# Performance work log

Measured on AMD Instinct MI355X. Metric: run time of the kernel, lower is better.

## Reference

```python
import jax, jax.numpy as jnp
import numpy as np

GROUP_SIZE = 128


def _unpack_int4(packed):
    # packed: [..., P] int32, each holding 8 int4 nibbles (LSB-first).
    u = jax.lax.bitcast_convert_type(packed, jnp.uint32)
    shifts = jnp.arange(8, dtype=jnp.uint32) * 4  # nibble bit offsets
    vals = (u[..., None] >> shifts) & jnp.uint32(15)  # [..., P, 8]
    return vals.reshape(*packed.shape[:-1], -1)  # [..., P*8] in [0, 15]


def setup_inputs() -> dict:
    key = jax.random.key(0)
    k1, k2, k3, k4 = jax.random.split(key, 4)
    B, S, K, O = 4, 16, 4096, 11008
    G = K // GROUP_SIZE          # 32 groups
    GP = (G + 7) // 8            # 4 packed-zero columns
    imax = np.iinfo(np.int32).max
    x = jax.random.normal(k1, (B, S, K), dtype=jnp.float16)
    qweight_i32 = jax.random.randint(k2, (O, K // 8), 0, imax, dtype=jnp.int32)
    qzeros_i32 = jax.random.randint(k3, (O, GP), 0, imax, dtype=jnp.int32)
    scales_f16 = jax.random.uniform(k4, (O, G), dtype=jnp.float16,
                                    minval=0.001, maxval=0.02)
    return {"x": x, "qweight_i32": qweight_i32, "qzeros_i32": qzeros_i32,
            "scales_f16": scales_f16}


def reference(x, qweight_i32, qzeros_i32, scales_f16):
    O, G = scales_f16.shape
    K = G * GROUP_SIZE
    # Dequantize: w = (q - z) * s, per-group int4 quantization.
    q = _unpack_int4(qweight_i32)[:, :K].astype(jnp.float16)       # [O, K]
    z = _unpack_int4(qzeros_i32)[:, :G].astype(jnp.float16)        # [O, G]
    z_k = jnp.repeat(z, GROUP_SIZE, axis=1)                        # [O, K]
    s_k = jnp.repeat(scales_f16, GROUP_SIZE, axis=1)               # [O, K]
    w = (q - z_k) * s_k                                            # fp16 [O, K]
    x2d = x.reshape(-1, K).astype(jnp.float16)                     # [m, K]
    out = jnp.matmul(x2d, w.T).astype(jnp.float32)                 # [m, O]
    return out.reshape(*x.shape[:-1], O)
```

## Files before the change

### kernel.cpp

```cpp
#include <hip/hip_runtime.h>
#include <stdint.h>

typedef _Float16 half8  __attribute__((ext_vector_type(8)));
typedef float    floatx4 __attribute__((ext_vector_type(4)));
typedef uint32_t uint4v  __attribute__((ext_vector_type(4)));

#define KDIM   4096
#define ODIM   11008
#define NG     32
#define KSPLIT 8
#define GPB    4
#define OBLK   172

__global__ void zero_out_kernel(float4* __restrict__ out) {
    out[(size_t)blockIdx.x * 256 + threadIdx.x] = float4{0.f, 0.f, 0.f, 0.f};
}

__device__ __forceinline__ uint32_t pk_f16(float a, float b) {
    return __builtin_bit_cast(uint32_t, __builtin_amdgcn_cvt_pkrtz(a, b));
}

__global__ __launch_bounds__(256) void cvt_x_kernel(
    const float4* __restrict__ x, uint4v* __restrict__ xh2,
    float* __restrict__ xsumT)
{
    const int i = blockIdx.x * 256 + threadIdx.x;
    const float4 f0 = x[2 * i];
    const float4 f1 = x[2 * i + 1];
    const uint4v v = {pk_f16(f0.x, f1.x), pk_f16(f0.y, f1.y),
                      pk_f16(f0.z, f1.z), pk_f16(f0.w, f1.w)};
    const int m  = i >> 9, c = i & 511;
    const int g  = c >> 4, cg = c & 15, q = cg >> 2, ks = cg & 3;
    const int mt = m >> 4, ml = m & 15;
    xh2[((size_t)(g * 4 + ks) * 4 + mt) * 64 + q * 16 + ml] = v;

    float p = f0.x + f0.y + f0.z + f0.w + f1.x + f1.y + f1.z + f1.w;
    p += __shfl_xor(p, 1);
    p += __shfl_xor(p, 2);
    p += __shfl_xor(p, 4);
    p += __shfl_xor(p, 8);
    if ((threadIdx.x & 15) == 0) xsumT[g * 64 + m] = p;
}

__global__ __launch_bounds__(256, 4) void w4a16_kernel(
    const uint4v*   __restrict__ xh2,
    const uint4v*   __restrict__ qw,
    const uint32_t* __restrict__ qz,
    const float*    __restrict__ sc,
    const float*    __restrict__ xsumT,
    float*          __restrict__ out)
{
    const int t    = threadIdx.x;
    const int wv   = t >> 6;
    const int lane = t & 63;
    const int q    = lane >> 4;
    const int ml   = lane & 15;

    const int ob = blockIdx.x % OBLK;
    const int kb = blockIdx.x / OBLK;
    const int o0 = ob * 64;
    const int g0 = kb * GPB;
    const int o  = o0 + wv * 16 + ml;

    const uint4v* qwp = qw + (size_t)o * 128 + g0 * 4 + q;
    uint4v u[GPB];
    #pragma unroll
    for (int g = 0; g < GPB; ++g) u[g] = qwp[g * 4];

    const uint32_t zdw  = qz[(size_t)o * 4 + (g0 >> 3)];
    const floatx4  svec = *reinterpret_cast<const floatx4*>(sc + (size_t)o * NG + g0);
    const int      zsh0 = (g0 & 7) * 4;

    const uint4v* xp = xh2 + (size_t)g0 * 1024 + lane;

    floatx4 acc[4] = {{0.f,0.f,0.f,0.f},{0.f,0.f,0.f,0.f},
                      {0.f,0.f,0.f,0.f},{0.f,0.f,0.f,0.f}};
    float czs[GPB];

    #pragma unroll
    for (int g = 0; g < GPB; ++g) {
        const uint32_t zn = (zdw >> (zsh0 + g * 4)) & 0xFu;
        const float    s  = svec[g];
        czs[g] = s * (1024.0f + (float)zn);

        floatx4 tmp[4] = {{0.f,0.f,0.f,0.f},{0.f,0.f,0.f,0.f},
                          {0.f,0.f,0.f,0.f},{0.f,0.f,0.f,0.f}};
        #pragma unroll
        for (int ks = 0; ks < 4; ++ks) {
            const uint32_t ud = u[g][ks];
            const uint4v bw = {
                ( ud         & 0x000F000Fu) | 0x64006400u,
                ((ud >> 4)   & 0x000F000Fu) | 0x64006400u,
                ((ud >> 8)   & 0x000F000Fu) | 0x64006400u,
                ((ud >> 12)  & 0x000F000Fu) | 0x64006400u};
            const half8 b = __builtin_bit_cast(half8, bw);
            #pragma unroll
            for (int mt = 0; mt < 4; ++mt) {
                const half8 a = __builtin_bit_cast(half8,
                    xp[(size_t)g * 1024 + ks * 256 + mt * 64]);
                tmp[mt] = __builtin_amdgcn_mfma_f32_16x16x32_f16(a, b, tmp[mt], 0, 0, 0);
            }
        }
        #pragma unroll
        for (int mt = 0; mt < 4; ++mt)
            #pragma unroll
            for (int r = 0; r < 4; ++r)
                acc[mt][r] += s * tmp[mt][r];
    }

    #pragma unroll
    for (int mt = 0; mt < 4; ++mt) {
        floatx4 corr = {0.f, 0.f, 0.f, 0.f};
        #pragma unroll
        for (int g = 0; g < GPB; ++g) {
            const floatx4 xs = *reinterpret_cast<const floatx4*>(
                xsumT + (g0 + g) * 64 + mt * 16 + q * 4);
            #pragma unroll
            for (int r = 0; r < 4; ++r) corr[r] += czs[g] * xs[r];
        }
        float* op = out + (size_t)(mt * 16 + q * 4) * ODIM + o;
        #pragma unroll
        for (int r = 0; r < 4; ++r)
            atomicAdd(op + (size_t)r * ODIM, acc[mt][r] - corr[r]);
    }
}

extern "C" void kernel_launch(void* const* d_in, const int* in_sizes, int n_in,
                              void* d_out, int out_size, void* d_ws, size_t ws_size,
                              hipStream_t stream) {
    const float*    x       = (const float*)d_in[0];
    const uint32_t* qweight = (const uint32_t*)d_in[1];
    const uint32_t* qzeros  = (const uint32_t*)d_in[2];
    const float*    scales  = (const float*)d_in[3];
    float* out = (float*)d_out;

    uint4v* xh2   = (uint4v*)d_ws;
    float*  xsumT = (float*)((char*)d_ws + 512 * 1024);

    cvt_x_kernel<<<dim3(128), dim3(256), 0, stream>>>((const float4*)x, xh2, xsumT);
    zero_out_kernel<<<dim3(688), dim3(256), 0, stream>>>((float4*)out);
    w4a16_kernel<<<dim3(OBLK * KSPLIT), dim3(256), 0, stream>>>(
        xh2, (const uint4v*)qweight, qzeros, scales, xsumT, out);
}
```

Baseline: 103.6 us.

## Replace global atomic split-K with in-block LDS reduction across waves

Each block now covers 16 output columns, and its 4 waves split K into 8 groups apiece. Partial sums are reduced through shared memory and written once with plain stores. This removes the zero-init kernel launch and the global atomicAdd traffic. It also software-prefetches the next weight vector, folds the zero-point correction into the group loop, and preloads activation fragments. The grid shrinks to 688 blocks with longer per-wave K loops, which may reduce parallelism and latency hiding.

```diff
diff --git a/kernel.cpp b/kernel.cpp
--- a/kernel.cpp
+++ b/kernel.cpp
@@ -5,16 +5,9 @@
 typedef float    floatx4 __attribute__((ext_vector_type(4)));
 typedef uint32_t uint4v  __attribute__((ext_vector_type(4)));
 
-#define KDIM   4096
-#define ODIM   11008
-#define NG     32
-#define KSPLIT 8
-#define GPB    4
-#define OBLK   172
-
-__global__ void zero_out_kernel(float4* __restrict__ out) {
-    out[(size_t)blockIdx.x * 256 + threadIdx.x] = float4{0.f, 0.f, 0.f, 0.f};
-}
+#define KDIM 4096
+#define ODIM 11008
+#define NG   32
 
 __device__ __forceinline__ uint32_t pk_f16(float a, float b) {
     return __builtin_bit_cast(uint32_t, __builtin_amdgcn_cvt_pkrtz(a, b));
@@ -50,44 +43,50 @@
     const float*    __restrict__ xsumT,
     float*          __restrict__ out)
 {
+    __shared__ float red[4][16][64];
+
     const int t    = threadIdx.x;
-    const int wv   = t >> 6;
+    const int kw   = t >> 6;
     const int lane = t & 63;
     const int q    = lane >> 4;
     const int ml   = lane & 15;
 
-    const int ob = blockIdx.x % OBLK;
-    const int kb = blockIdx.x / OBLK;
-    const int o0 = ob * 64;
-    const int g0 = kb * GPB;
-    const int o  = o0 + wv * 16 + ml;
+    const int o0 = blockIdx.x * 16;
+    const int o  = o0 + ml;
+    const int g0 = kw * 8;
 
     const uint4v* qwp = qw + (size_t)o * 128 + g0 * 4 + q;
-    uint4v u[GPB];
-    #pragma unroll
-    for (int g = 0; g < GPB; ++g) u[g] = qwp[g * 4];
-
-    const uint32_t zdw  = qz[(size_t)o * 4 + (g0 >> 3)];
-    const floatx4  svec = *reinterpret_cast<const floatx4*>(sc + (size_t)o * NG + g0);
-    const int      zsh0 = (g0 & 7) * 4;
+    const uint32_t zdw = qz[(size_t)o * 4 + kw];
+    const floatx4 sv0 = *reinterpret_cast<const floatx4*>(sc + (size_t)o * NG + g0);
+    const floatx4 sv1 = *reinterpret_cast<const floatx4*>(sc + (size_t)o * NG + g0 + 4);
 
     const uint4v* xp = xh2 + (size_t)g0 * 1024 + lane;
+    const float*  xs = xsumT + (size_t)g0 * 64 + q * 4;
 
     floatx4 acc[4] = {{0.f,0.f,0.f,0.f},{0.f,0.f,0.f,0.f},
                       {0.f,0.f,0.f,0.f},{0.f,0.f,0.f,0.f}};
-    float czs[GPB];
+
+    uint4v ucur = qwp[0];
 
     #pragma unroll
-    for (int g = 0; g < GPB; ++g) {
-        const uint32_t zn = (zdw >> (zsh0 + g * 4)) & 0xFu;
-        const float    s  = svec[g];
-        czs[g] = s * (1024.0f + (float)zn);
+    for (int gl = 0; gl < 8; ++gl) {
+        uint4v unext;
+        if (gl + 1 < 8) unext = qwp[(gl + 1) * 4];
+
+        const uint32_t zn  = (zdw >> (gl * 4)) & 0xFu;
+        const float    s   = (gl < 4) ? sv0[gl] : sv1[gl - 4];
+        const float    czs = s * (1024.0f + (float)zn);
 
         floatx4 tmp[4] = {{0.f,0.f,0.f,0.f},{0.f,0.f,0.f,0.f},
                           {0.f,0.f,0.f,0.f},{0.f,0.f,0.f,0.f}};
         #pragma unroll
         for (int ks = 0; ks < 4; ++ks) {
-            const uint32_t ud = u[g][ks];
+            uint4v ax[4];
+            #pragma unroll
+            for (int mt = 0; mt < 4; ++mt)
+                ax[mt] = xp[(size_t)(gl * 16 + ks * 4 + mt) * 64];
+
+            const uint32_t ud = ucur[ks];
             const uint4v bw = {
                 ( ud         & 0x000F000Fu) | 0x64006400u,
                 ((ud >> 4)   & 0x000F000Fu) | 0x64006400u,
@@ -95,33 +94,36 @@
                 ((ud >> 12)  & 0x000F000Fu) | 0x64006400u};
             const half8 b = __builtin_bit_cast(half8, bw);
             #pragma unroll
-            for (int mt = 0; mt < 4; ++mt) {
-                const half8 a = __builtin_bit_cast(half8,
-                    xp[(size_t)g * 1024 + ks * 256 + mt * 64]);
-                tmp[mt] = __builtin_amdgcn_mfma_f32_16x16x32_f16(a, b, tmp[mt], 0, 0, 0);
-            }
+            for (int mt = 0; mt < 4; ++mt)
+                tmp[mt] = __builtin_amdgcn_mfma_f32_16x16x32_f16(
+                    __builtin_bit_cast(half8, ax[mt]), b, tmp[mt], 0, 0, 0);
         }
+
         #pragma unroll
-        for (int mt = 0; mt < 4; ++mt)
+        for (int mt = 0; mt < 4; ++mt) {
+            const floatx4 xg = *reinterpret_cast<const floatx4*>(
+                xs + gl * 64 + mt * 16);
             #pragma unroll
             for (int r = 0; r < 4; ++r)
-                acc[mt][r] += s * tmp[mt][r];
+                acc[mt][r] += s * tmp[mt][r] - czs * xg[r];
+        }
+        ucur = unext;
     }
 
     #pragma unroll
-    for (int mt = 0; mt < 4; ++mt) {
-        floatx4 corr = {0.f, 0.f, 0.f, 0.f};
-        #pragma unroll
-        for (int g = 0; g < GPB; ++g) {
-            const floatx4 xs = *reinterpret_cast<const floatx4*>(
-                xsumT + (g0 + g) * 64 + mt * 16 + q * 4);
-            #pragma unroll
-            for (int r = 0; r < 4; ++r) corr[r] += czs[g] * xs[r];
-        }
-        float* op = out + (size_t)(mt * 16 + q * 4) * ODIM + o;
+    for (int mt = 0; mt < 4; ++mt)
         #pragma unroll
         for (int r = 0; r < 4; ++r)
-            atomicAdd(op + (size_t)r * ODIM, acc[mt][r] - corr[r]);
+            red[kw][mt * 4 + r][lane] = acc[mt][r];
+    __syncthreads();
+
+    const int mt2 = t >> 6;
+    #pragma unroll
+    for (int r = 0; r < 4; ++r) {
+        const int i = mt2 * 4 + r;
+        const float sum = red[0][i][lane] + red[1][i][lane]
+                        + red[2][i][lane] + red[3][i][lane];
+        out[(size_t)(mt2 * 16 + q * 4 + r) * ODIM + o] = sum;
     }
 }
 
@@ -138,7 +140,6 @@
     float*  xsumT = (float*)((char*)d_ws + 512 * 1024);
 
     cvt_x_kernel<<<dim3(128), dim3(256), 0, stream>>>((const float4*)x, xh2, xsumT);
-    zero_out_kernel<<<dim3(688), dim3(256), 0, stream>>>((float4*)out);
-    w4a16_kernel<<<dim3(OBLK * KSPLIT), dim3(256), 0, stream>>>(
+    w4a16_kernel<<<dim3(ODIM / 16), dim3(256), 0, stream>>>(
         xh2, (const uint4v*)qweight, qzeros, scales, xsumT, out);
 }
```

Result: slower. 111.0 us (+7.2%).
